# Kernel optimization log

Measured on AMD Instinct MI355X. Metric: run time of the kernel, lower is better.

Reference implementation:

```python
import jax, jax.numpy as jnp
import numpy as np

NUM_HEADS = 16
HEAD_DIM = 64
COMP_RATIO = 8


def setup_inputs() -> dict:
    key = jax.random.key(0)
    ks = jax.random.split(key, 6)
    d_model = NUM_HEADS * HEAD_DIM  # 1024
    B, S = 2, 8192
    scale = 1.0 / np.sqrt(d_model)
    x = jax.random.normal(ks[0], (B, S, d_model), dtype=jnp.float32)
    Wq = jax.random.normal(ks[1], (d_model, NUM_HEADS * HEAD_DIM), dtype=jnp.float32) * scale
    Wk = jax.random.normal(ks[2], (d_model, NUM_HEADS * HEAD_DIM), dtype=jnp.float32) * scale
    Wv = jax.random.normal(ks[3], (d_model, NUM_HEADS * HEAD_DIM), dtype=jnp.float32) * scale
    Wo = jax.random.normal(ks[4], (NUM_HEADS * HEAD_DIM, d_model), dtype=jnp.float32) * scale
    bq = jnp.zeros((NUM_HEADS * HEAD_DIM,), jnp.float32)
    bk = jnp.zeros((NUM_HEADS * HEAD_DIM,), jnp.float32)
    bv = jnp.zeros((NUM_HEADS * HEAD_DIM,), jnp.float32)
    bo = jnp.zeros((d_model,), jnp.float32)
    return {"x": x, "local_window_start": 4096, "Wq": Wq, "bq": bq,
            "Wk": Wk, "bk": bk, "Wv": Wv, "bv": bv, "Wo": Wo, "bo": bo}


def reference(x, local_window_start, Wq, bq, Wk, bk, Wv, bv, Wo, bo):
    B, S, D = x.shape
    H, Hd, R = NUM_HEADS, HEAD_DIM, COMP_RATIO
    if local_window_start <= R:
        return jnp.zeros_like(x)
    num_pools = local_window_start // R
    if num_pools == 0:
        return jnp.zeros_like(x)
    trunc = num_pools * R
    # avg-pool compression of tokens before the local window
    compressed = x[:, :trunc, :].reshape(B, num_pools, R, D).mean(axis=2)  # (B, P, D)
    # projections
    q = (x @ Wq + bq).reshape(B, S, H, Hd).transpose(0, 2, 1, 3)            # (B,H,S,Hd)
    k = (compressed @ Wk + bk).reshape(B, num_pools, H, Hd).transpose(0, 2, 1, 3)  # (B,H,P,Hd)
    v = (compressed @ Wv + bv).reshape(B, num_pools, H, Hd).transpose(0, 2, 1, 3)
    scale = 1.0 / jnp.sqrt(jnp.float32(Hd))
    scores = jnp.einsum('bhqd,bhkd->bhqk', q, k) * scale                    # (B,H,S,P)
    # causal mask: a query can attend to a pool only if the pool fully precedes it
    q_pos = jnp.arange(S)[:, None]
    pool_end = (jnp.arange(num_pools) + 1) * R
    mask = q_pos >= pool_end[None, :]                                       # (S, P)
    scores = jnp.where(mask[None, None], scores, -1e9)
    attn = jax.nn.softmax(scores, axis=-1)
    out = jnp.einsum('bhqk,bhkd->bhqd', attn, v)                            # (B,H,S,Hd)
    out = out.transpose(0, 2, 1, 3).reshape(B, S, H * Hd)
    return out @ Wo + bo
```

## Files before the change

### kernel.cpp

```cpp
#include <hip/hip_runtime.h>
#include <hip/hip_bf16.h>


typedef __attribute__((ext_vector_type(8))) short bf16x8;
typedef __attribute__((ext_vector_type(4))) short bf16x4;
typedef __attribute__((ext_vector_type(4))) float f32x4;

#define MFMA_BF16(a, b, c) __builtin_amdgcn_mfma_f32_16x16x32_bf16((a), (b), (c), 0, 0, 0)

__device__ __forceinline__ unsigned short f2bu(float x) {
  __hip_bfloat16 b = __float2bfloat16(x);
  return __builtin_bit_cast(unsigned short, b);
}

__device__ __forceinline__ unsigned cvtpk(float lo, float hi) {
  unsigned r;
  asm("v_cvt_pk_bf16_f32 %0, %1, %2" : "=v"(r) : "v"(lo), "v"(hi));
  return r;
}

__device__ __forceinline__ float fexp2(float x) {
  float r;
  asm("v_exp_f32 %0, %1" : "=v"(r) : "v"(x));
  return r;
}

__device__ __forceinline__ void gload_lds16(const void* g, void* l) {
  __builtin_amdgcn_global_load_lds(
      (const __attribute__((address_space(1))) unsigned*)(g),
      (__attribute__((address_space(3))) unsigned*)(l), 16, 0, 0);
}

__device__ __forceinline__ unsigned ldsaddr(const void* p) {
  return (unsigned)(unsigned long long)(const __attribute__((address_space(3))) char*)p;
}

__global__ void prep_kernel(const float* __restrict__ x,
                            __hip_bfloat16* __restrict__ xb,
                            __hip_bfloat16* __restrict__ cb,
                            const float* __restrict__ w0, const float* __restrict__ w1,
                            const float* __restrict__ w2, const float* __restrict__ w3,
                            __hip_bfloat16* __restrict__ t0, __hip_bfloat16* __restrict__ t1,
                            __hip_bfloat16* __restrict__ t2, __hip_bfloat16* __restrict__ t3) {
  __shared__ float tile[32][33];
  const int bid = blockIdx.x;
  const int tid = threadIdx.x;
  if (bid < 2048) {
    const int b = bid >> 10, g = bid & 1023;
    const int d = tid * 4;
    const size_t rb = ((size_t)(b * 8192 + g * 8)) * 1024 + d;
    float4 a = {0.f, 0.f, 0.f, 0.f};
#pragma unroll
    for (int r = 0; r < 8; ++r) {
      const float4 v = *(const float4*)&x[rb + (size_t)r * 1024];
      ushort4 o;
      o.x = f2bu(v.x); o.y = f2bu(v.y); o.z = f2bu(v.z); o.w = f2bu(v.w);
      *(ushort4*)&xb[rb + (size_t)r * 1024] = o;
      a.x += v.x; a.y += v.y; a.z += v.z; a.w += v.w;
    }
    if (g < 512) {
      ushort4 o;
      o.x = f2bu(a.x * 0.125f); o.y = f2bu(a.y * 0.125f);
      o.z = f2bu(a.z * 0.125f); o.w = f2bu(a.w * 0.125f);
      *(ushort4*)&cb[((size_t)(b * 512 + g)) * 1024 + d] = o;
    }
  } else {
    const int t = bid - 2048;
    const int z = t >> 10, rem = t & 1023;
    const int k0 = (rem & 31) * 32, n0 = (rem >> 5) * 32;
    const float* W; __hip_bfloat16* T;
    switch (z) {
      case 0: W = w0; T = t0; break;
      case 1: W = w1; T = t1; break;
      case 2: W = w2; T = t2; break;
      default: W = w3; T = t3; break;
    }
    const int tx = tid & 31, ty = tid >> 5;
#pragma unroll
    for (int j = 0; j < 4; ++j) {
      const int kk = ty + j * 8;
      tile[kk][tx] = W[(size_t)(k0 + kk) * 1024 + n0 + tx];
    }
    __syncthreads();
#pragma unroll
    for (int j = 0; j < 4; ++j) {
      const int nn = ty + j * 8;
      T[(size_t)(n0 + nn) * 1024 + k0 + tx] = __float2bfloat16(tile[tx][nn]);
    }
  }
}


#define STAGE(SPTR, SROWBASE, STILE, SLDSOFF)                                  \
  {                                                                            \
    const int _t = (STILE) < NT ? (STILE) : 0;                                 \
    const size_t _kb = (size_t)_t * 128;                                       \
    gload_lds16((const char*)(SPTR) + ((size_t)((SROWBASE) + srow0) * K) * 2 + _kb + scb0, \
                ldsC + (SLDSOFF) + wave * 1024);                               \
    gload_lds16((const char*)(SPTR) + ((size_t)((SROWBASE) + srow0 + 64) * K) * 2 + _kb + scb0, \
                ldsC + (SLDSOFF) + 8192 + wave * 1024);                        \
  }

#define MM4(MR, AF0, AF1)                                                      \
  acc[MR][0] = MFMA_BF16(AF0, bf00, acc[MR][0]);                               \
  acc[MR][1] = MFMA_BF16(AF0, bf10, acc[MR][1]);                               \
  acc[MR][2] = MFMA_BF16(AF0, bf20, acc[MR][2]);                               \
  acc[MR][3] = MFMA_BF16(AF0, bf30, acc[MR][3]);                               \
  acc[MR][0] = MFMA_BF16(AF1, bf01, acc[MR][0]);                               \
  acc[MR][1] = MFMA_BF16(AF1, bf11, acc[MR][1]);                               \
  acc[MR][2] = MFMA_BF16(AF1, bf21, acc[MR][2]);                               \
  acc[MR][3] = MFMA_BF16(AF1, bf31, acc[MR][3]);

#define PHASE(QM, DB, LOADB, SPTR, SROWBASE, STILE, SLDSOFF, DOVM)             \
  {                                                                            \
    bf16x8 af0, af1, af2, af3;                                                 \
    const unsigned ab = Ab0 + (DB)*32768u + (QM)*4096u;                        \
    asm volatile("ds_read_b128 %0, %1" : "=v"(af0) : "v"(ab));                 \
    asm volatile("ds_read_b128 %0, %1" : "=v"(af1) : "v"(ab ^ 64u));           \
    asm volatile("ds_read_b128 %0, %1" : "=v"(af2) : "v"(ab + 2048u));         \
    asm volatile("ds_read_b128 %0, %1" : "=v"(af3) : "v"((ab + 2048u) ^ 64u)); \
    if (LOADB) {                                                               \
      const unsigned bb = Bb0 + (DB)*32768u;                                   \
      asm volatile("ds_read_b128 %0, %1" : "=v"(bf00) : "v"(bb));              \
      asm volatile("ds_read_b128 %0, %1" : "=v"(bf01) : "v"(bb ^ 64u));        \
      asm volatile("ds_read_b128 %0, %1" : "=v"(bf10) : "v"(bb + 2048u));      \
      asm volatile("ds_read_b128 %0, %1" : "=v"(bf11) : "v"((bb + 2048u) ^ 64u)); \
      asm volatile("ds_read_b128 %0, %1" : "=v"(bf20) : "v"(bb + 4096u));      \
      asm volatile("ds_read_b128 %0, %1" : "=v"(bf21) : "v"((bb + 4096u) ^ 64u)); \
      asm volatile("ds_read_b128 %0, %1" : "=v"(bf30) : "v"(bb + 6144u));      \
      asm volatile("ds_read_b128 %0, %1" : "=v"(bf31) : "v"((bb + 6144u) ^ 64u)); \
    }                                                                          \
    STAGE(SPTR, SROWBASE, STILE, SLDSOFF)                                      \
    asm volatile("s_barrier" ::: "memory");                                    \
    asm volatile("s_waitcnt lgkmcnt(0)" ::: "memory");                         \
    __builtin_amdgcn_sched_barrier(0);                                         \
    __builtin_amdgcn_s_setprio(1);                                             \
    MM4((QM)*2 + 0, af0, af1)                                                  \
    MM4((QM)*2 + 1, af2, af3)                                                  \
    __builtin_amdgcn_s_setprio(0);                                             \
    if (DOVM) asm volatile("s_waitcnt vmcnt(4)" ::: "memory");                 \
    asm volatile("s_barrier" ::: "memory");                                    \
  }

template <typename OUT_T>
__global__ __launch_bounds__(512, 2) void gemm256_kernel(
    const __hip_bfloat16* __restrict__ A, const __hip_bfloat16* __restrict__ Bt,
    const float* __restrict__ bias, OUT_T* __restrict__ C, int M, int N, int K) {
  __shared__ alignas(16) char lds[131072];
  char* ldsC = lds;
  const int tid = threadIdx.x;
  const int wave = tid >> 6, lane = tid & 63;
  const int l15 = lane & 15, lg = lane >> 4;
  const int wm = wave >> 2, wn = wave & 3;

  const int nwg = gridDim.x, cpx = nwg >> 3;
  const int bid = blockIdx.x;
  const int swz = (bid & 7) * cpx + (bid >> 3);
  const int ncol = N >> 8;
  const int bn = swz % ncol, bm = swz / ncol;
  const long brow = (long)bm * 256;
  const long bcol = (long)bn * 256;

  const int NT = K >> 6;
  const int NITER = K >> 7;

  const int o0 = wave * 1024 + lane * 16;
  const int srow0 = o0 >> 7;
  const int scb0 = (o0 & 127) ^ ((srow0 & 7) << 4);

  const unsigned LB = ldsaddr(lds);
  const int off0 = (lg * 16) ^ ((l15 & 7) << 4);
  const unsigned Ab0 = LB + wm * 16384u + l15 * 128u + off0;
  const unsigned Bb0 = LB + 65536u + (wn >> 1) * 16384u + (wn & 1) * 8192u + l15 * 128u + off0;

  f32x4 acc[8][4];
#pragma unroll
  for (int m = 0; m < 8; ++m)
#pragma unroll
    for (int n = 0; n < 4; ++n) acc[m][n] = (f32x4){0.f, 0.f, 0.f, 0.f};

  bf16x8 bf00, bf01, bf10, bf11, bf20, bf21, bf30, bf31;

  STAGE(Bt, bcol + 128, 0, 81920)
  STAGE(Bt, bcol,       0, 65536)
  STAGE(A,  brow,       0, 0)
  STAGE(A,  brow + 128, 0, 16384)
  STAGE(Bt, bcol + 128, 1, 114688)
  STAGE(Bt, bcol,       1, 98304)
  asm volatile("s_waitcnt vmcnt(4)" ::: "memory");
  asm volatile("s_barrier" ::: "memory");

  for (int i = 0; i < NITER; ++i) {
    const int t0 = 2 * i;
    PHASE(0, 0, true,  A,  brow,       t0 + 1, 32768,  false)
    PHASE(1, 0, false, A,  brow + 128, t0 + 1, 49152,  false)
    PHASE(2, 0, false, Bt, bcol + 128, t0 + 2, 81920,  false)
    PHASE(3, 0, false, Bt, bcol,       t0 + 2, 65536,  true)
    PHASE(0, 1, true,  A,  brow,       t0 + 2, 0,      false)
    PHASE(1, 1, false, A,  brow + 128, t0 + 2, 16384,  false)
    PHASE(2, 1, false, Bt, bcol + 128, t0 + 3, 114688, false)
    PHASE(3, 1, false, Bt, bcol,       t0 + 3, 98304,  true)
  }

#pragma unroll
  for (int nn = 0; nn < 4; ++nn) {
    const long col = bcol + wn * 64 + nn * 16 + l15;
    const float bv = bias[col];
#pragma unroll
    for (int mr = 0; mr < 8; ++mr) {
      const long row = brow + wm * 128 + mr * 16 + lg * 4;
#pragma unroll
      for (int j = 0; j < 4; ++j) {
        const float v = acc[mr][nn][j] + bv;
        if constexpr (sizeof(OUT_T) == 2)
          C[(row + j) * N + col] = __float2bfloat16(v);
        else
          C[(row + j) * N + col] = v;
      }
    }
  }
}

__global__ __launch_bounds__(256, 2) void gemm_bt_dual_kernel(
    const __hip_bfloat16* __restrict__ A,
    const __hip_bfloat16* __restrict__ Bt0, const float* __restrict__ b0,
    __hip_bfloat16* __restrict__ C0,
    const __hip_bfloat16* __restrict__ Bt1, const float* __restrict__ b1,
    __hip_bfloat16* __restrict__ Vt, int M, int N, int K) {
  const int sel = blockIdx.x >= (unsigned)(N >> 7);
  const __hip_bfloat16* Bt = sel ? Bt1 : Bt0;
  const float* bias = sel ? b1 : b0;
  const int bx = blockIdx.x - sel * (N >> 7);

  __shared__ alignas(16) __hip_bfloat16 As[128 * 32];
  __shared__ alignas(16) __hip_bfloat16 Bs[128 * 32];
  const int tid = threadIdx.x;
  const int wave = tid >> 6, lane = tid & 63;
  const int l15 = lane & 15, lg = lane >> 4;
  const long brow = (long)blockIdx.y * 128;
  const long bcol = (long)bx * 128;
  const int wr = (wave >> 1) * 64;
  const int wc = (wave & 1) * 64;

  f32x4 acc[4][4];
#pragma unroll
  for (int m = 0; m < 4; ++m)
#pragma unroll
    for (int n = 0; n < 4; ++n) acc[m][n] = (f32x4){0.f, 0.f, 0.f, 0.f};

  for (int kt = 0; kt < K; kt += 32) {
#pragma unroll
    for (int j = 0; j < 2; ++j) {
      const int seg = wave * 2 + j;
      const int o = seg * 1024;
      const int ob = o + lane * 16;
      const int row = ob >> 6;
      const int cb = ob & 63;
      gload_lds16((const char*)A + ((brow + row) * (long)K + kt) * 2 + cb, (char*)As + o);
      gload_lds16((const char*)Bt + ((bcol + row) * (long)K + kt) * 2 + cb, (char*)Bs + o);
    }
    __syncthreads();
    bf16x8 af[4], bfr[4];
#pragma unroll
    for (int m = 0; m < 4; ++m)
      af[m] = *(const bf16x8*)&As[(wr + m * 16 + l15) * 32 + lg * 8];
#pragma unroll
    for (int n = 0; n < 4; ++n)
      bfr[n] = *(const bf16x8*)&Bs[(wc + n * 16 + l15) * 32 + lg * 8];
#pragma unroll
    for (int m = 0; m < 4; ++m)
#pragma unroll
      for (int n = 0; n < 4; ++n)
        acc[m][n] = MFMA_BF16(af[m], bfr[n], acc[m][n]);
    __syncthreads();
  }

#pragma unroll
  for (int m = 0; m < 4; ++m)
#pragma unroll
    for (int n = 0; n < 4; ++n) {
      const long col = bcol + wc + n * 16 + l15;
      const float bv = bias[col];
      const long row0 = brow + wr + m * 16 + lg * 4;
      if (!sel) {
#pragma unroll
        for (int r = 0; r < 4; ++r)
          C0[(row0 + r) * N + col] = __float2bfloat16(acc[m][n][r] + bv);
      } else {
        const int bb = (int)(row0 >> 9);
        const int p = (int)(row0 & 511);
        ushort4 w;
        w.x = f2bu(acc[m][n][0] + bv);
        w.y = f2bu(acc[m][n][1] + bv);
        w.z = f2bu(acc[m][n][2] + bv);
        w.w = f2bu(acc[m][n][3] + bv);
        *(ushort4*)&Vt[((size_t)(bb * 1024 + col)) * 512 + p] = w;
      }
    }
}

__global__ __launch_bounds__(512, 2) void attn_kernel(
    const __hip_bfloat16* __restrict__ Q,
    const __hip_bfloat16* __restrict__ Km,
    const __hip_bfloat16* __restrict__ Vt,
    __hip_bfloat16* __restrict__ O) {
  __shared__ alignas(16) __hip_bfloat16 Ks[512 * 64];
  __shared__ alignas(16) __hip_bfloat16 VT[64 * 512];
  const int bh = blockIdx.x;
  const int b = bh >> 4, h = bh & 15;
  const int tid = threadIdx.x, wave = tid >> 6, lane = tid & 63;
  const int l15 = lane & 15, lg = lane >> 4;
  const char* Kbase = (const char*)(Km + (size_t)b * 512 * 1024 + h * 64);
  const char* VtP = (const char*)(Vt + (size_t)bh * 32768);
  char* KsB = (char*)Ks;
  char* VTB = (char*)VT;

#pragma unroll
  for (int j = 0; j < 8; ++j) {
    const int seg = wave * 8 + j;
    const int p = seg * 8 + (lane >> 3);
    const int cb = ((lane & 7) * 16) ^ ((p & 7) << 4);
    gload_lds16(Kbase + (size_t)p * 2048 + cb, KsB + seg * 1024);
  }
#pragma unroll
  for (int j = 0; j < 8; ++j) {
    const int d = wave * 8 + j;
    const int cb = (lane * 16) ^ ((d & 7) << 4);
    gload_lds16(VtP + (size_t)d * 1024 + cb, VTB + d * 1024);
  }
  __syncthreads();

  constexpr float SC = 0.18033688011112042f;
  for (int itq = 0; itq < 4; ++itq) {
    const int y = blockIdx.y;
    const int sidx = (itq == 0) ? y : (itq == 1) ? 15 - y
                   : (itq == 2) ? 16 + y : 31 - y;
    const int q0 = sidx * 256 + wave * 32;
    const __hip_bfloat16* Qr0 = Q + ((size_t)(b * 8192 + q0 + l15)) * 1024 + h * 64;
    const __hip_bfloat16* Qr1 = Qr0 + (size_t)16 * 1024;
    const bf16x8 qa0 = *(const bf16x8*)(Qr0 + lg * 8);
    const bf16x8 qa1 = *(const bf16x8*)(Qr0 + 32 + lg * 8);
    const bf16x8 qb0 = *(const bf16x8*)(Qr1 + lg * 8);
    const bf16x8 qb1 = *(const bf16x8*)(Qr1 + 32 + lg * 8);

    float l0 = 0.f, l1 = 0.f;
    f32x4 o4[2][4];
#pragma unroll
    for (int g = 0; g < 2; ++g)
#pragma unroll
      for (int d = 0; d < 4; ++d) o4[g][d] = (f32x4){0.f, 0.f, 0.f, 0.f};

#pragma unroll
    for (int ch = 0; ch < 4; ++ch) {
      if (!(ch == 0 || q0 == 0 || q0 >= ch * 1024)) continue;

      f32x4 s[2][8];
      __builtin_amdgcn_s_setprio(1);
#pragma unroll
      for (int cc = 0; cc < 8; ++cc) {
        const int p = ch * 128 + cc * 16 + l15;
        const int rb = p * 128;
        const int sw = (p & 7) << 4;
        const bf16x8 kf0 = *(const bf16x8*)(KsB + rb + ((lg * 16) ^ sw));
        const bf16x8 kf1 = *(const bf16x8*)(KsB + rb + ((lg * 16 + 64) ^ sw));
        f32x4 z0 = {0.f, 0.f, 0.f, 0.f};
        z0 = MFMA_BF16(kf0, qa0, z0);
        z0 = MFMA_BF16(kf1, qa1, z0);
        s[0][cc] = z0;
        f32x4 z1 = {0.f, 0.f, 0.f, 0.f};
        z1 = MFMA_BF16(kf0, qb0, z1);
        z1 = MFMA_BF16(kf1, qb1, z1);
        s[1][cc] = z1;
      }
      __builtin_amdgcn_s_setprio(0);
      if (q0 < (ch + 1) * 1024) {
#pragma unroll
        for (int g = 0; g < 2; ++g) {
          const int qa = q0 + g * 16 + l15;
          const float mval = (qa >= 8) ? -1.0e9f : 0.f;
#pragma unroll
          for (int cc = 0; cc < 8; ++cc) {
            const int pb8 = (ch * 128 + cc * 16 + lg * 4 + 1) * 8;
#pragma unroll
            for (int r = 0; r < 4; ++r)
              if (qa < pb8 + r * 8) s[g][cc][r] = mval;
          }
        }
      }
#pragma unroll
      for (int cc = 0; cc < 8; ++cc)
#pragma unroll
        for (int r = 0; r < 4; ++r) {
          const float e0 = fexp2(s[0][cc][r] * SC);
          const float e1 = fexp2(s[1][cc][r] * SC);
          s[0][cc][r] = e0; l0 += e0;
          s[1][cc][r] = e1; l1 += e1;
        }
#pragma unroll
      for (int kc = 0; kc < 4; ++kc) {
        uint4 u0, u1;
        u0.x = cvtpk(s[0][kc * 2][0], s[0][kc * 2][1]);
        u0.y = cvtpk(s[0][kc * 2][2], s[0][kc * 2][3]);
        u0.z = cvtpk(s[0][kc * 2 + 1][0], s[0][kc * 2 + 1][1]);
        u0.w = cvtpk(s[0][kc * 2 + 1][2], s[0][kc * 2 + 1][3]);
        u1.x = cvtpk(s[1][kc * 2][0], s[1][kc * 2][1]);
        u1.y = cvtpk(s[1][kc * 2][2], s[1][kc * 2][3]);
        u1.z = cvtpk(s[1][kc * 2 + 1][0], s[1][kc * 2 + 1][1]);
        u1.w = cvtpk(s[1][kc * 2 + 1][2], s[1][kc * 2 + 1][3]);
        const bf16x8 p0 = __builtin_bit_cast(bf16x8, u0);
        const bf16x8 p1 = __builtin_bit_cast(bf16x8, u1);
        const int pbase = ch * 128 + kc * 32;
        __builtin_amdgcn_s_setprio(1);
#pragma unroll
        for (int db = 0; db < 4; ++db) {
          const int d = db * 16 + l15;
          const int rowb = d * 1024;
          const int sw = (d & 7) << 4;
          const bf16x4 v0 = *(const bf16x4*)(VTB + rowb + (((pbase + lg * 4) * 2) ^ sw));
          const bf16x4 v1 = *(const bf16x4*)(VTB + rowb + (((pbase + 16 + lg * 4) * 2) ^ sw));
          const bf16x8 af = {v0[0], v0[1], v0[2], v0[3], v1[0], v1[1], v1[2], v1[3]};
          o4[0][db] = MFMA_BF16(af, p0, o4[0][db]);
          o4[1][db] = MFMA_BF16(af, p1, o4[1][db]);
        }
        __builtin_amdgcn_s_setprio(0);
      }
    }
#pragma unroll
    for (int g = 0; g < 2; ++g) {
      float t = g ? l1 : l0;
      t += __shfl_xor(t, 16);
      t += __shfl_xor(t, 32);
      const float inv = 1.f / t;
      __hip_bfloat16* Op =
          O + ((size_t)(b * 8192 + q0 + g * 16 + l15)) * 1024 + h * 64 + lg * 4;
#pragma unroll
      for (int db = 0; db < 4; ++db) {
        uint2 w;
        w.x = cvtpk(o4[g][db][0] * inv, o4[g][db][1] * inv);
        w.y = cvtpk(o4[g][db][2] * inv, o4[g][db][3] * inv);
        *(uint2*)(Op + db * 16) = w;
      }
    }
  }
}

extern "C" void kernel_launch(void* const* d_in, const int* in_sizes, int n_in,
                              void* d_out, int out_size, void* d_ws, size_t ws_size,
                              hipStream_t stream) {
  const float* x  = (const float*)d_in[0];
  const float* Wq = (const float*)d_in[2];
  const float* bq = (const float*)d_in[3];
  const float* Wk = (const float*)d_in[4];
  const float* bk = (const float*)d_in[5];
  const float* Wv = (const float*)d_in[6];
  const float* bv = (const float*)d_in[7];
  const float* Wo = (const float*)d_in[8];
  const float* bo = (const float*)d_in[9];
  float* out = (float*)d_out;

  constexpr size_t SZ_XB = (size_t)16384 * 1024 * 2;
  constexpr size_t SZ_WT = (size_t)1024 * 1024 * 2;
  constexpr size_t SZ_CB = (size_t)1024 * 1024 * 2;
  char* ws = (char*)d_ws;
  __hip_bfloat16* xb   = (__hip_bfloat16*)ws;
  __hip_bfloat16* WqT  = (__hip_bfloat16*)(ws + SZ_XB);
  __hip_bfloat16* WkT  = (__hip_bfloat16*)(ws + SZ_XB + SZ_WT);
  __hip_bfloat16* WvT  = (__hip_bfloat16*)(ws + SZ_XB + 2 * SZ_WT);
  __hip_bfloat16* WoT  = (__hip_bfloat16*)(ws + SZ_XB + 3 * SZ_WT);
  __hip_bfloat16* cbuf = (__hip_bfloat16*)(ws + SZ_XB + 4 * SZ_WT);
  __hip_bfloat16* Qb   = (__hip_bfloat16*)(ws + SZ_XB + 4 * SZ_WT + SZ_CB);
  __hip_bfloat16* Kb   = (__hip_bfloat16*)(ws + SZ_XB + 4 * SZ_WT + SZ_CB + SZ_XB);
  __hip_bfloat16* Vtb  = (__hip_bfloat16*)(ws + SZ_XB + 4 * SZ_WT + SZ_CB + SZ_XB + SZ_CB);

  prep_kernel<<<dim3(6144), dim3(256), 0, stream>>>(
      x, xb, cbuf, Wq, Wk, Wv, Wo, WqT, WkT, WvT, WoT);
  gemm256_kernel<__hip_bfloat16><<<dim3(256), dim3(512), 0, stream>>>(
      xb, WqT, bq, Qb, 16384, 1024, 1024);
  gemm_bt_dual_kernel<<<dim3(16, 8), dim3(256), 0, stream>>>(
      cbuf, WkT, bk, Kb, WvT, bv, Vtb, 1024, 1024, 1024);
  attn_kernel<<<dim3(32, 8), dim3(512), 0, stream>>>(Qb, Kb, Vtb, xb);
  gemm256_kernel<float><<<dim3(256), dim3(512), 0, stream>>>(
      xb, WoT, bo, out, 16384, 1024, 1024);
}
```

Measured before the change: 170.8 us.

## Process 64 queries per wave with interleaved per-32-pool QK/softmax/PV steps

Each wave now handles 64 query rows (4 groups of 16) instead of 32, so every K and V fragment read from LDS feeds twice as many MFMAs. The score, mask, exp and PV work is done in 32-pool steps rather than whole 128-pool chunks, which keeps the live score registers small. The query loop drops from 4 to 2 iterations, and launch bounds change to one block per SIMD group to allow more registers per thread. The setprio hints are removed. The risk is lower occupancy and a different tail balance across blocks.

Result: slower. 176.0 us (+3.1%).

```diff
diff --git a/kernel.cpp b/kernel.cpp
--- a/kernel.cpp
+++ b/kernel.cpp
@@ -299,7 +299,7 @@
     }
 }
 
-__global__ __launch_bounds__(512, 2) void attn_kernel(
+__global__ __launch_bounds__(512, 1) void attn_kernel(
     const __hip_bfloat16* __restrict__ Q,
     const __hip_bfloat16* __restrict__ Km,
     const __hip_bfloat16* __restrict__ Vt,
@@ -331,86 +331,80 @@
   __syncthreads();
 
   constexpr float SC = 0.18033688011112042f;
-  for (int itq = 0; itq < 4; ++itq) {
-    const int y = blockIdx.y;
-    const int sidx = (itq == 0) ? y : (itq == 1) ? 15 - y
-                   : (itq == 2) ? 16 + y : 31 - y;
-    const int q0 = sidx * 256 + wave * 32;
-    const __hip_bfloat16* Qr0 = Q + ((size_t)(b * 8192 + q0 + l15)) * 1024 + h * 64;
-    const __hip_bfloat16* Qr1 = Qr0 + (size_t)16 * 1024;
-    const bf16x8 qa0 = *(const bf16x8*)(Qr0 + lg * 8);
-    const bf16x8 qa1 = *(const bf16x8*)(Qr0 + 32 + lg * 8);
-    const bf16x8 qb0 = *(const bf16x8*)(Qr1 + lg * 8);
-    const bf16x8 qb1 = *(const bf16x8*)(Qr1 + 32 + lg * 8);
-
-    float l0 = 0.f, l1 = 0.f;
-    f32x4 o4[2][4];
-#pragma unroll
-    for (int g = 0; g < 2; ++g)
+  for (int itq = 0; itq < 2; ++itq) {
+    const int sidx = itq == 0 ? blockIdx.y : 15 - blockIdx.y;
+    const int q0 = sidx * 512 + wave * 64;
+
+    bf16x8 qf[4][2];
+#pragma unroll
+    for (int g = 0; g < 4; ++g) {
+      const __hip_bfloat16* Qr =
+          Q + ((size_t)(b * 8192 + q0 + g * 16 + l15)) * 1024 + h * 64;
+      qf[g][0] = *(const bf16x8*)(Qr + lg * 8);
+      qf[g][1] = *(const bf16x8*)(Qr + 32 + lg * 8);
+    }
+
+    float lsum[4] = {0.f, 0.f, 0.f, 0.f};
+    f32x4 o4[4][4];
+#pragma unroll
+    for (int g = 0; g < 4; ++g)
 #pragma unroll
       for (int d = 0; d < 4; ++d) o4[g][d] = (f32x4){0.f, 0.f, 0.f, 0.f};
 
 #pragma unroll
     for (int ch = 0; ch < 4; ++ch) {
       if (!(ch == 0 || q0 == 0 || q0 >= ch * 1024)) continue;
-
-      f32x4 s[2][8];
-      __builtin_amdgcn_s_setprio(1);
-#pragma unroll
-      for (int cc = 0; cc < 8; ++cc) {
-        const int p = ch * 128 + cc * 16 + l15;
-        const int rb = p * 128;
-        const int sw = (p & 7) << 4;
-        const bf16x8 kf0 = *(const bf16x8*)(KsB + rb + ((lg * 16) ^ sw));
-        const bf16x8 kf1 = *(const bf16x8*)(KsB + rb + ((lg * 16 + 64) ^ sw));
-        f32x4 z0 = {0.f, 0.f, 0.f, 0.f};
-        z0 = MFMA_BF16(kf0, qa0, z0);
-        z0 = MFMA_BF16(kf1, qa1, z0);
-        s[0][cc] = z0;
-        f32x4 z1 = {0.f, 0.f, 0.f, 0.f};
-        z1 = MFMA_BF16(kf0, qb0, z1);
-        z1 = MFMA_BF16(kf1, qb1, z1);
-        s[1][cc] = z1;
-      }
-      __builtin_amdgcn_s_setprio(0);
-      if (q0 < (ch + 1) * 1024) {
-#pragma unroll
-        for (int g = 0; g < 2; ++g) {
-          const int qa = q0 + g * 16 + l15;
-          const float mval = (qa >= 8) ? -1.0e9f : 0.f;
-#pragma unroll
-          for (int cc = 0; cc < 8; ++cc) {
-            const int pb8 = (ch * 128 + cc * 16 + lg * 4 + 1) * 8;
-#pragma unroll
-            for (int r = 0; r < 4; ++r)
-              if (qa < pb8 + r * 8) s[g][cc][r] = mval;
+      const bool bnd = q0 < (ch + 1) * 1024;
+
+#pragma unroll
+      for (int kc = 0; kc < 4; ++kc) {
+        f32x4 s[4][2];
+#pragma unroll
+        for (int c2 = 0; c2 < 2; ++c2) {
+          const int p = ch * 128 + (kc * 2 + c2) * 16 + l15;
+          const int rb = p * 128;
+          const int sw = (p & 7) << 4;
+          const bf16x8 kf0 = *(const bf16x8*)(KsB + rb + ((lg * 16) ^ sw));
+          const bf16x8 kf1 = *(const bf16x8*)(KsB + rb + ((lg * 16 + 64) ^ sw));
+#pragma unroll
+          for (int g = 0; g < 4; ++g) {
+            f32x4 z = {0.f, 0.f, 0.f, 0.f};
+            z = MFMA_BF16(kf0, qf[g][0], z);
+            z = MFMA_BF16(kf1, qf[g][1], z);
+            s[g][c2] = z;
           }
         }
-      }
-#pragma unroll
-      for (int cc = 0; cc < 8; ++cc)
-#pragma unroll
-        for (int r = 0; r < 4; ++r) {
-          const float e0 = fexp2(s[0][cc][r] * SC);
-          const float e1 = fexp2(s[1][cc][r] * SC);
-          s[0][cc][r] = e0; l0 += e0;
-          s[1][cc][r] = e1; l1 += e1;
+        if (bnd) {
+#pragma unroll
+          for (int g = 0; g < 4; ++g) {
+            const int qa = q0 + g * 16 + l15;
+            const float mval = (qa >= 8) ? -1.0e9f : 0.f;
+#pragma unroll
+            for (int c2 = 0; c2 < 2; ++c2) {
+              const int pb8 = (ch * 128 + (kc * 2 + c2) * 16 + lg * 4 + 1) * 8;
+#pragma unroll
+              for (int r = 0; r < 4; ++r)
+                if (qa < pb8 + r * 8) s[g][c2][r] = mval;
+            }
+          }
         }
-#pragma unroll
-      for (int kc = 0; kc < 4; ++kc) {
-        uint4 u0, u1;
-        u0.x = cvtpk(s[0][kc * 2][0], s[0][kc * 2][1]);
-        u0.y = cvtpk(s[0][kc * 2][2], s[0][kc * 2][3]);
-        u0.z = cvtpk(s[0][kc * 2 + 1][0], s[0][kc * 2 + 1][1]);
-        u0.w = cvtpk(s[0][kc * 2 + 1][2], s[0][kc * 2 + 1][3]);
-        u1.x = cvtpk(s[1][kc * 2][0], s[1][kc * 2][1]);
-        u1.y = cvtpk(s[1][kc * 2][2], s[1][kc * 2][3]);
-        u1.z = cvtpk(s[1][kc * 2 + 1][0], s[1][kc * 2 + 1][1]);
-        u1.w = cvtpk(s[1][kc * 2 + 1][2], s[1][kc * 2 + 1][3]);
-        const bf16x8 p0 = __builtin_bit_cast(bf16x8, u0);
-        const bf16x8 p1 = __builtin_bit_cast(bf16x8, u1);
+        uint4 pk[4];
+#pragma unroll
+        for (int g = 0; g < 4; ++g) {
+#pragma unroll
+          for (int c2 = 0; c2 < 2; ++c2)
+#pragma unroll
+            for (int r = 0; r < 4; ++r) {
+              const float e = fexp2(s[g][c2][r] * SC);
+              s[g][c2][r] = e;
+              lsum[g] += e;
+            }
+          pk[g].x = cvtpk(s[g][0][0], s[g][0][1]);
+          pk[g].y = cvtpk(s[g][0][2], s[g][0][3]);
+          pk[g].z = cvtpk(s[g][1][0], s[g][1][1]);
+          pk[g].w = cvtpk(s[g][1][2], s[g][1][3]);
+        }
         const int pbase = ch * 128 + kc * 32;
-        __builtin_amdgcn_s_setprio(1);
 #pragma unroll
         for (int db = 0; db < 4; ++db) {
           const int d = db * 16 + l15;
@@ -419,15 +413,15 @@
           const bf16x4 v0 = *(const bf16x4*)(VTB + rowb + (((pbase + lg * 4) * 2) ^ sw));
           const bf16x4 v1 = *(const bf16x4*)(VTB + rowb + (((pbase + 16 + lg * 4) * 2) ^ sw));
           const bf16x8 af = {v0[0], v0[1], v0[2], v0[3], v1[0], v1[1], v1[2], v1[3]};
-          o4[0][db] = MFMA_BF16(af, p0, o4[0][db]);
-          o4[1][db] = MFMA_BF16(af, p1, o4[1][db]);
+#pragma unroll
+          for (int g = 0; g < 4; ++g)
+            o4[g][db] = MFMA_BF16(af, __builtin_bit_cast(bf16x8, pk[g]), o4[g][db]);
         }
-        __builtin_amdgcn_s_setprio(0);
       }
     }
 #pragma unroll
-    for (int g = 0; g < 2; ++g) {
-      float t = g ? l1 : l0;
+    for (int g = 0; g < 4; ++g) {
+      float t = lsum[g];
       t += __shfl_xor(t, 16);
       t += __shfl_xor(t, 32);
       const float inv = 1.f / t;
```

## Fold softmax scale into Q projection and compute row sums via MFMA

Applied to the files above, without the earlier changes.

Moves the softmax scale (log2e/sqrt(d)) into the Q-projection GEMM epilogue, so the attention kernel applies exp2 directly to the scores without a multiply. The softmax denominator is now accumulated with an MFMA against a ones vector on the bf16 probabilities, which replaces the scalar adds and the cross-lane shuffle reduction. The s_setprio hints in the attention loop are also removed. The trade-off is extra MFMA work, a denominator summed from bf16-rounded probabilities, and Q stored pre-scaled in bf16, which slightly changes the rounding.

After: 162.3 us. 1.05x faster.

```diff
diff --git a/kernel.cpp b/kernel.cpp
--- a/kernel.cpp
+++ b/kernel.cpp
@@ -145,7 +145,8 @@
 template <typename OUT_T>
 __global__ __launch_bounds__(512, 2) void gemm256_kernel(
     const __hip_bfloat16* __restrict__ A, const __hip_bfloat16* __restrict__ Bt,
-    const float* __restrict__ bias, OUT_T* __restrict__ C, int M, int N, int K) {
+    const float* __restrict__ bias, OUT_T* __restrict__ C, int M, int N, int K,
+    float oscale) {
   __shared__ alignas(16) char lds[131072];
   char* ldsC = lds;
   const int tid = threadIdx.x;
@@ -211,7 +212,7 @@
       const long row = brow + wm * 128 + mr * 16 + lg * 4;
 #pragma unroll
       for (int j = 0; j < 4; ++j) {
-        const float v = acc[mr][nn][j] + bv;
+        const float v = (acc[mr][nn][j] + bv) * oscale;
         if constexpr (sizeof(OUT_T) == 2)
           C[(row + j) * N + col] = __float2bfloat16(v);
         else
@@ -330,7 +331,10 @@
   }
   __syncthreads();
 
-  constexpr float SC = 0.18033688011112042f;
+  const short one_bf = (short)0x3F80;
+  const bf16x8 ones = {one_bf, one_bf, one_bf, one_bf,
+                       one_bf, one_bf, one_bf, one_bf};
+
   for (int itq = 0; itq < 4; ++itq) {
     const int y = blockIdx.y;
     const int sidx = (itq == 0) ? y : (itq == 1) ? 15 - y
@@ -343,7 +347,7 @@
     const bf16x8 qb0 = *(const bf16x8*)(Qr1 + lg * 8);
     const bf16x8 qb1 = *(const bf16x8*)(Qr1 + 32 + lg * 8);
 
-    float l0 = 0.f, l1 = 0.f;
+    f32x4 lac0 = {0.f, 0.f, 0.f, 0.f}, lac1 = {0.f, 0.f, 0.f, 0.f};
     f32x4 o4[2][4];
 #pragma unroll
     for (int g = 0; g < 2; ++g)
@@ -355,7 +359,6 @@
       if (!(ch == 0 || q0 == 0 || q0 >= ch * 1024)) continue;
 
       f32x4 s[2][8];
-      __builtin_amdgcn_s_setprio(1);
 #pragma unroll
       for (int cc = 0; cc < 8; ++cc) {
         const int p = ch * 128 + cc * 16 + l15;
@@ -372,7 +375,6 @@
         z1 = MFMA_BF16(kf1, qb1, z1);
         s[1][cc] = z1;
       }
-      __builtin_amdgcn_s_setprio(0);
       if (q0 < (ch + 1) * 1024) {
 #pragma unroll
         for (int g = 0; g < 2; ++g) {
@@ -391,10 +393,8 @@
       for (int cc = 0; cc < 8; ++cc)
 #pragma unroll
         for (int r = 0; r < 4; ++r) {
-          const float e0 = fexp2(s[0][cc][r] * SC);
-          const float e1 = fexp2(s[1][cc][r] * SC);
-          s[0][cc][r] = e0; l0 += e0;
-          s[1][cc][r] = e1; l1 += e1;
+          s[0][cc][r] = fexp2(s[0][cc][r]);
+          s[1][cc][r] = fexp2(s[1][cc][r]);
         }
 #pragma unroll
       for (int kc = 0; kc < 4; ++kc) {
@@ -409,8 +409,9 @@
         u1.w = cvtpk(s[1][kc * 2 + 1][2], s[1][kc * 2 + 1][3]);
         const bf16x8 p0 = __builtin_bit_cast(bf16x8, u0);
         const bf16x8 p1 = __builtin_bit_cast(bf16x8, u1);
+        lac0 = MFMA_BF16(ones, p0, lac0);
+        lac1 = MFMA_BF16(ones, p1, lac1);
         const int pbase = ch * 128 + kc * 32;
-        __builtin_amdgcn_s_setprio(1);
 #pragma unroll
         for (int db = 0; db < 4; ++db) {
           const int d = db * 16 + l15;
@@ -422,15 +423,11 @@
           o4[0][db] = MFMA_BF16(af, p0, o4[0][db]);
           o4[1][db] = MFMA_BF16(af, p1, o4[1][db]);
         }
-        __builtin_amdgcn_s_setprio(0);
       }
     }
 #pragma unroll
     for (int g = 0; g < 2; ++g) {
-      float t = g ? l1 : l0;
-      t += __shfl_xor(t, 16);
-      t += __shfl_xor(t, 32);
-      const float inv = 1.f / t;
+      const float inv = 1.f / (g ? lac1[0] : lac0[0]);
       __hip_bfloat16* Op =
           O + ((size_t)(b * 8192 + q0 + g * 16 + l15)) * 1024 + h * 64 + lg * 4;
 #pragma unroll
@@ -472,13 +469,15 @@
   __hip_bfloat16* Kb   = (__hip_bfloat16*)(ws + SZ_XB + 4 * SZ_WT + SZ_CB + SZ_XB);
   __hip_bfloat16* Vtb  = (__hip_bfloat16*)(ws + SZ_XB + 4 * SZ_WT + SZ_CB + SZ_XB + SZ_CB);
 
+  constexpr float SC = 0.18033688011112042f;
+
   prep_kernel<<<dim3(6144), dim3(256), 0, stream>>>(
       x, xb, cbuf, Wq, Wk, Wv, Wo, WqT, WkT, WvT, WoT);
   gemm256_kernel<__hip_bfloat16><<<dim3(256), dim3(512), 0, stream>>>(
-      xb, WqT, bq, Qb, 16384, 1024, 1024);
+      xb, WqT, bq, Qb, 16384, 1024, 1024, SC);
   gemm_bt_dual_kernel<<<dim3(16, 8), dim3(256), 0, stream>>>(
       cbuf, WkT, bk, Kb, WvT, bv, Vtb, 1024, 1024, 1024);
   attn_kernel<<<dim3(32, 8), dim3(512), 0, stream>>>(Qb, Kb, Vtb, xb);
   gemm256_kernel<float><<<dim3(256), dim3(512), 0, stream>>>(
-      xb, WoT, bo, out, 16384, 1024, 1024);
-}
+      xb, WoT, bo, out, 16384, 1024, 1024, 1.0f);
+}
```
